# Kernel tuning notes

Measured on AMD Instinct MI355X. Metric: run time of the kernel, lower is better.

Reference implementation:

```python
import jax, jax.numpy as jnp
import numpy as np


def _masked_var(x, mask):
    # unbiased variance (torch.var default, ddof=1) over entries where mask==1
    cnt = jnp.sum(mask)
    mean = jnp.sum(x * mask) / jnp.maximum(cnt, 1.0)
    return jnp.sum(mask * (x - mean) ** 2) / jnp.maximum(cnt - 1.0, 1.0)


def setup_inputs() -> dict:
    key = jax.random.key(0)
    ks = jax.random.split(key, 9)
    B, N, F = 4, 8192, 64
    points = jax.random.normal(ks[0], (B, N, 3), dtype=jnp.float32)
    features = jax.random.normal(ks[1], (B, N, F), dtype=jnp.float32)
    leaf_mask = jax.random.randint(ks[2], (B, N), 0, 2).astype(bool)
    W1 = jax.random.normal(ks[3], (64, F + 3), dtype=jnp.float32) * 0.05
    b1 = jax.random.normal(ks[4], (64,), dtype=jnp.float32) * 0.05
    W2 = jax.random.normal(ks[5], (32, 64), dtype=jnp.float32) * 0.05
    b2 = jax.random.normal(ks[6], (32,), dtype=jnp.float32) * 0.05
    W3 = jax.random.normal(ks[7], (1, 32), dtype=jnp.float32) * 0.05
    b3 = jax.random.normal(ks[8], (1,), dtype=jnp.float32) * 0.05
    return {"points": points, "features": features, "leaf_mask": leaf_mask,
            "W1": W1, "b1": b1, "W2": W2, "b2": b2, "W3": W3, "b3": b3}


def reference(points, features, leaf_mask, W1, b1, W2, b2, W3, b3):
    # NOTE: in the original Torch code combined_feat = [feat(F), xyz(3), var(1)]
    # (length F+4) is truncated to expected_input_dim = F+3, so the kNN feature
    # variance is provably dropped. The MLP input is exactly [feat, xyz].
    B, N, _ = points.shape

    def mlp(x):  # x: [N, F+3]
        h = jax.nn.relu(x @ W1.T + b1)
        h = jax.nn.relu(h @ W2.T + b2)
        return jax.nn.sigmoid(h @ W3.T + b3)[:, 0]

    def per_batch(pts, feats, mask):
        maskf = mask.astype(pts.dtype)
        x = jnp.concatenate([feats, pts], axis=-1)  # [N, F+3]
        scores = mlp(x) * maskf  # non-leaf points stay 0
        n_leaf = jnp.sum(maskf)
        scores = jnp.where(n_leaf < 10.0, jnp.zeros_like(scores), scores)

        # separation confidence
        clarity = _masked_var(scores, maskf)
        sel = scores > 0.7
        cnt = jnp.sum(sel.astype(jnp.int32))
        idx = jnp.arange(N)
        order = jnp.argsort(jnp.where(sel, idx, N + idx))  # selected first, in order
        g = pts[order]  # [N,3]
        d = jnp.linalg.norm(g[1:] - g[:-1], axis=1)  # consecutive boundary-point dists
        pair_mask = (jnp.arange(N - 1) < cnt - 1).astype(pts.dtype)
        dvar = _masked_var(d, pair_mask)
        cont = jnp.clip(1.0 / (dvar + 1e-8), 0.0, 1.0)
        cont = jnp.where(cnt > 5, cont, 0.0)
        conf = jnp.clip(clarity * cont, 0.0, 1.0)
        conf = jnp.where(n_leaf == 0.0, 0.0, conf)
        return scores, conf

    boundary_prob, separation_confidence = jax.vmap(per_batch)(points, features, leaf_mask)
    return boundary_prob, features, separation_confidence
```

## Files before the change

### kernel.cpp

```cpp
#include <hip/hip_runtime.h>
#include <math.h>

#define NB 4
#define NPTS 8192
#define OUT_FEAT_OFF 32768
#define OUT_CONF_OFF (32768 + 2097152)

__device__ __forceinline__ float blockReduceSum256(float v) {
    __shared__ float sred[4];
#pragma unroll
    for (int o = 32; o > 0; o >>= 1) v += __shfl_down(v, o, 64);
    const int w = threadIdx.x >> 6, l = threadIdx.x & 63;
    __syncthreads();
    if (l == 0) sred[w] = v;
    __syncthreads();
    return sred[0] + sred[1] + sred[2] + sred[3];
}

__global__ __launch_bounds__(256) void fused_kernel(
    const float* __restrict__ pts,
    const float* __restrict__ feats,
    const int* __restrict__ mask,
    const float* __restrict__ W1,
    const float* __restrict__ b1,
    const float* __restrict__ W2,
    const float* __restrict__ b2,
    const float* __restrict__ W3,
    const float* __restrict__ b3,
    float* __restrict__ out,
    int* __restrict__ counters,
    float* __restrict__ wsf)
{
    __shared__ float sX[64 * 68];
    __shared__ float sH[3 * 64 * 36];
    __shared__ int sflag;
    __shared__ int cnts[256];

    const int t = threadIdx.x;
    const int ln = t & 63;
    const int q = __builtin_amdgcn_readfirstlane(t >> 6);

    {
        const float4* fsrc = (const float4*)feats + (size_t)blockIdx.x * 1024;
        float4* fdst = (float4*)(out + OUT_FEAT_OFF) + (size_t)blockIdx.x * 1024;
#pragma unroll
        for (int i = 0; i < 4; ++i) {
            const int e = i * 256 + t;
            const float4 v = fsrc[e];
            fdst[e] = v;
            *(float4*)&sX[(e >> 4) * 68 + (e & 15) * 4] = v;
        }
    }
    __syncthreads();

    const int p = blockIdx.x * 64 + ln;

    float4 xv[16];
#pragma unroll
    for (int kc = 0; kc < 16; ++kc)
        xv[kc] = *(const float4*)&sX[ln * 68 + kc * 4];
    const float px = pts[(size_t)p * 3 + 0];
    const float py = pts[(size_t)p * 3 + 1];
    const float pz = pts[(size_t)p * 3 + 2];

    const int jq = q * 16;
    float h1[16];
#pragma unroll
    for (int jj = 0; jj < 16; ++jj) {
        const float* wr = W1 + (size_t)(jq + jj) * 67;
        float a = b1[jq + jj];
#pragma unroll
        for (int kc = 0; kc < 16; ++kc) {
            a = fmaf(xv[kc].x, wr[4 * kc + 0], a);
            a = fmaf(xv[kc].y, wr[4 * kc + 1], a);
            a = fmaf(xv[kc].z, wr[4 * kc + 2], a);
            a = fmaf(xv[kc].w, wr[4 * kc + 3], a);
        }
        a = fmaf(px, wr[64], a);
        a = fmaf(py, wr[65], a);
        a = fmaf(pz, wr[66], a);
        h1[jj] = fmaxf(a, 0.f);
    }

    float p2[32];
#pragma unroll
    for (int j = 0; j < 32; ++j) {
        const float* wr = W2 + (size_t)j * 64 + jq;
        float a = 0.f;
#pragma unroll
        for (int kk = 0; kk < 16; ++kk) a = fmaf(h1[kk], wr[kk], a);
        p2[j] = a;
    }

    if (q != 0) {
        float* dst = &sH[(size_t)((q - 1) * 64 + ln) * 36];
#pragma unroll
        for (int m = 0; m < 8; ++m) {
            float4 v;
            v.x = p2[4 * m + 0]; v.y = p2[4 * m + 1];
            v.z = p2[4 * m + 2]; v.w = p2[4 * m + 3];
            *(float4*)&dst[4 * m] = v;
        }
    }
    __syncthreads();

    if (q == 0) {
#pragma unroll
        for (int qq = 0; qq < 3; ++qq) {
            const float* src = &sH[(size_t)(qq * 64 + ln) * 36];
#pragma unroll
            for (int m = 0; m < 8; ++m) {
                const float4 v = *(const float4*)&src[4 * m];
                p2[4 * m + 0] += v.x; p2[4 * m + 1] += v.y;
                p2[4 * m + 2] += v.z; p2[4 * m + 3] += v.w;
            }
        }
        float z = b3[0];
#pragma unroll
        for (int j = 0; j < 32; ++j)
            z = fmaf(fmaxf(p2[j] + b2[j], 0.f), W3[j], z);
        float sc = 1.0f / (1.0f + expf(-z));
        if (mask[p] == 0) sc = 0.0f;
        out[p] = sc;
    }

    const int batch = blockIdx.x >> 7;
    __syncthreads();
    if (t == 0) {
        const int old = __hip_atomic_fetch_add(&counters[batch], 1,
                                               __ATOMIC_ACQ_REL,
                                               __HIP_MEMORY_SCOPE_AGENT);
        sflag = (old == 127);
    }
    __syncthreads();
    if (!sflag) return;
    __builtin_amdgcn_fence(__ATOMIC_ACQUIRE, "agent");

    float* scores = out + (size_t)batch * NPTS;
    const float* P = pts + (size_t)batch * NPTS * 3;
    const int* M = mask + (size_t)batch * NPTS;
    float* g = wsf + (size_t)batch * 40960;
    float* dd = g + 3 * NPTS;

    float s[32];
    unsigned int mbits = 0;
#pragma unroll
    for (int i = 0; i < 8; ++i) {
        const float4 s4 = ((const float4*)scores)[t * 8 + i];
        s[4*i+0] = s4.x; s[4*i+1] = s4.y; s[4*i+2] = s4.z; s[4*i+3] = s4.w;
        const int4 m4 = ((const int4*)M)[t * 8 + i];
        mbits |= (m4.x != 0 ? 1u : 0u) << (4*i+0);
        mbits |= (m4.y != 0 ? 1u : 0u) << (4*i+1);
        mbits |= (m4.z != 0 ? 1u : 0u) << (4*i+2);
        mbits |= (m4.w != 0 ? 1u : 0u) << (4*i+3);
    }

    float ss = 0.f;
#pragma unroll
    for (int i = 0; i < 32; ++i) ss += s[i];
    const float nleaf = blockReduceSum256((float)__popc(mbits));
    const float ssum = blockReduceSum256(ss);

    if (nleaf < 10.0f) {
        const float4 z4 = {0.f, 0.f, 0.f, 0.f};
#pragma unroll
        for (int i = 0; i < 8; ++i) ((float4*)scores)[t * 8 + i] = z4;
        if (t == 0) out[OUT_CONF_OFF + batch] = 0.0f;
        return;
    }

    const float mean = ssum / fmaxf(nleaf, 1.0f);
    float vs = 0.f;
#pragma unroll
    for (int i = 0; i < 32; ++i) {
        if (mbits & (1u << i)) {
            const float d0 = s[i] - mean;
            vs += d0 * d0;
        }
    }
    const float clarity = blockReduceSum256(vs) / fmaxf(nleaf - 1.0f, 1.0f);

    int c0 = 0;
#pragma unroll
    for (int i = 0; i < 32; ++i) c0 += (s[i] > 0.7f);
    cnts[t] = c0;
    __syncthreads();
    for (int off = 1; off < 256; off <<= 1) {
        const int v = cnts[t];
        const int a = (t >= off) ? cnts[t - off] : 0;
        __syncthreads();
        cnts[t] = v + a;
        __syncthreads();
    }
    const int cnt = cnts[255];
    int pos = cnts[t] - c0;
#pragma unroll
    for (int i = 0; i < 32; ++i) {
        if (s[i] > 0.7f) {
            const int idx = t * 32 + i;
            g[3 * pos + 0] = P[3 * idx + 0];
            g[3 * pos + 1] = P[3 * idx + 1];
            g[3 * pos + 2] = P[3 * idx + 2];
            ++pos;
        }
    }
    __syncthreads();

    const int npair = cnt - 1;
    float dsum = 0.f;
    for (int i = t; i < npair; i += 256) {
        const float ax = g[3 * i + 0] - g[3 * i + 3];
        const float ay = g[3 * i + 1] - g[3 * i + 4];
        const float az = g[3 * i + 2] - g[3 * i + 5];
        const float d0 = sqrtf(ax * ax + ay * ay + az * az);
        dd[i] = d0;
        dsum += d0;
    }
    const float dtot = blockReduceSum256(dsum);
    const float npf = (float)npair;
    const float dmean = dtot / fmaxf(npf, 1.0f);
    float dv = 0.f;
    for (int i = t; i < npair; i += 256) {
        const float e = dd[i] - dmean;
        dv += e * e;
    }
    const float dvar = blockReduceSum256(dv) / fmaxf(npf - 1.0f, 1.0f);

    float cont = fminf(fmaxf(1.0f / (dvar + 1e-8f), 0.0f), 1.0f);
    if (!(cnt > 5)) cont = 0.0f;
    const float conf = fminf(fmaxf(clarity * cont, 0.0f), 1.0f);
    if (t == 0) out[OUT_CONF_OFF + batch] = conf;
}

extern "C" void kernel_launch(void* const* d_in, const int* in_sizes, int n_in,
                              void* d_out, int out_size, void* d_ws, size_t ws_size,
                              hipStream_t stream) {
    const float* points   = (const float*)d_in[0];
    const float* features = (const float*)d_in[1];
    const int*   leafmask = (const int*)d_in[2];
    const float* W1 = (const float*)d_in[3];
    const float* b1 = (const float*)d_in[4];
    const float* W2 = (const float*)d_in[5];
    const float* b2 = (const float*)d_in[6];
    const float* W3 = (const float*)d_in[7];
    const float* b3 = (const float*)d_in[8];
    float* out = (float*)d_out;
    int* counters = (int*)d_ws;
    float* wsf = (float*)d_ws + 64;

    (void)hipMemsetAsync(d_ws, 0, 64, stream);
    fused_kernel<<<512, 256, 0, stream>>>(
        points, features, leafmask, W1, b1, W2, b2, W3, b3, out, counters, wsf);
}
```

Before: 117.0 us.

## Use wave-shuffle scan, LDS distance buffer, and split FMA accumulators

The per-batch tail block's shared-memory Hillis-Steele prefix scan, which needed many __syncthreads, is replaced by a wave-level __shfl_up scan plus a small cross-wave combine. Consecutive-point distances now go to LDS, reusing the MLP staging buffer, instead of a global workspace. The MLP dot products use several independent accumulators to shorten FMA dependency chains. The point coordinate loads are hoisted ahead of the feature copy, and launch bounds now request two blocks per SM. Splitting the accumulators changes the floating-point summation order, and the occupancy hint may limit how many registers the compiler can use.

New measurement: 109.6 us. -6.3%, faster.

```diff
diff --git a/kernel.cpp b/kernel.cpp
--- a/kernel.cpp
+++ b/kernel.cpp
@@ -17,7 +17,7 @@
     return sred[0] + sred[1] + sred[2] + sred[3];
 }
 
-__global__ __launch_bounds__(256) void fused_kernel(
+__global__ __launch_bounds__(256, 2) void fused_kernel(
     const float* __restrict__ pts,
     const float* __restrict__ feats,
     const int* __restrict__ mask,
@@ -31,14 +31,21 @@
     int* __restrict__ counters,
     float* __restrict__ wsf)
 {
-    __shared__ float sX[64 * 68];
-    __shared__ float sH[3 * 64 * 36];
+    __shared__ float smem[11264];
+    float* const sX = smem;
+    float* const sH = smem + 64 * 68;
     __shared__ int sflag;
-    __shared__ int cnts[256];
+    __shared__ int swt[4];
 
     const int t = threadIdx.x;
     const int ln = t & 63;
     const int q = __builtin_amdgcn_readfirstlane(t >> 6);
+
+    const int p = blockIdx.x * 64 + ln;
+
+    const float px = pts[(size_t)p * 3 + 0];
+    const float py = pts[(size_t)p * 3 + 1];
+    const float pz = pts[(size_t)p * 3 + 2];
 
     {
         const float4* fsrc = (const float4*)feats + (size_t)blockIdx.x * 1024;
@@ -53,43 +60,41 @@
     }
     __syncthreads();
 
-    const int p = blockIdx.x * 64 + ln;
-
     float4 xv[16];
 #pragma unroll
     for (int kc = 0; kc < 16; ++kc)
         xv[kc] = *(const float4*)&sX[ln * 68 + kc * 4];
-    const float px = pts[(size_t)p * 3 + 0];
-    const float py = pts[(size_t)p * 3 + 1];
-    const float pz = pts[(size_t)p * 3 + 2];
 
     const int jq = q * 16;
     float h1[16];
 #pragma unroll
     for (int jj = 0; jj < 16; ++jj) {
-        const float* wr = W1 + (size_t)(jq + jj) * 67;
-        float a = b1[jq + jj];
+        const float* __restrict__ wr = W1 + (size_t)(jq + jj) * 67;
+        float a0 = b1[jq + jj], a1 = 0.f, a2 = 0.f, a3 = 0.f;
 #pragma unroll
         for (int kc = 0; kc < 16; ++kc) {
-            a = fmaf(xv[kc].x, wr[4 * kc + 0], a);
-            a = fmaf(xv[kc].y, wr[4 * kc + 1], a);
-            a = fmaf(xv[kc].z, wr[4 * kc + 2], a);
-            a = fmaf(xv[kc].w, wr[4 * kc + 3], a);
-        }
-        a = fmaf(px, wr[64], a);
-        a = fmaf(py, wr[65], a);
-        a = fmaf(pz, wr[66], a);
-        h1[jj] = fmaxf(a, 0.f);
+            a0 = fmaf(xv[kc].x, wr[4 * kc + 0], a0);
+            a1 = fmaf(xv[kc].y, wr[4 * kc + 1], a1);
+            a2 = fmaf(xv[kc].z, wr[4 * kc + 2], a2);
+            a3 = fmaf(xv[kc].w, wr[4 * kc + 3], a3);
+        }
+        a0 = fmaf(px, wr[64], a0);
+        a1 = fmaf(py, wr[65], a1);
+        a2 = fmaf(pz, wr[66], a2);
+        h1[jj] = fmaxf((a0 + a1) + (a2 + a3), 0.f);
     }
 
     float p2[32];
 #pragma unroll
     for (int j = 0; j < 32; ++j) {
-        const float* wr = W2 + (size_t)j * 64 + jq;
-        float a = 0.f;
-#pragma unroll
-        for (int kk = 0; kk < 16; ++kk) a = fmaf(h1[kk], wr[kk], a);
-        p2[j] = a;
+        const float* __restrict__ wr = W2 + (size_t)j * 64 + jq;
+        float a0 = 0.f, a1 = 0.f;
+#pragma unroll
+        for (int kk = 0; kk < 8; ++kk) {
+            a0 = fmaf(h1[2 * kk + 0], wr[2 * kk + 0], a0);
+            a1 = fmaf(h1[2 * kk + 1], wr[2 * kk + 1], a1);
+        }
+        p2[j] = a0 + a1;
     }
 
     if (q != 0) {
@@ -140,7 +145,6 @@
     const float* P = pts + (size_t)batch * NPTS * 3;
     const int* M = mask + (size_t)batch * NPTS;
     float* g = wsf + (size_t)batch * 40960;
-    float* dd = g + 3 * NPTS;
 
     float s[32];
     unsigned int mbits = 0;
@@ -183,17 +187,23 @@
     int c0 = 0;
 #pragma unroll
     for (int i = 0; i < 32; ++i) c0 += (s[i] > 0.7f);
-    cnts[t] = c0;
-    __syncthreads();
-    for (int off = 1; off < 256; off <<= 1) {
-        const int v = cnts[t];
-        const int a = (t >= off) ? cnts[t - off] : 0;
-        __syncthreads();
-        cnts[t] = v + a;
-        __syncthreads();
-    }
-    const int cnt = cnts[255];
-    int pos = cnts[t] - c0;
+    int incl = c0;
+#pragma unroll
+    for (int o = 1; o < 64; o <<= 1) {
+        const int u = __shfl_up(incl, o, 64);
+        if (ln >= o) incl += u;
+    }
+    const int w = t >> 6;
+    if (ln == 63) swt[w] = incl;
+    __syncthreads();
+    int woff = 0, cnt = 0;
+#pragma unroll
+    for (int i = 0; i < 4; ++i) {
+        const int wv = swt[i];
+        if (i < w) woff += wv;
+        cnt += wv;
+    }
+    int pos = woff + (incl - c0);
 #pragma unroll
     for (int i = 0; i < 32; ++i) {
         if (s[i] > 0.7f) {
@@ -206,22 +216,25 @@
     }
     __syncthreads();
 
+    float* const ddl = smem;
     const int npair = cnt - 1;
     float dsum = 0.f;
+#pragma unroll 4
     for (int i = t; i < npair; i += 256) {
         const float ax = g[3 * i + 0] - g[3 * i + 3];
         const float ay = g[3 * i + 1] - g[3 * i + 4];
         const float az = g[3 * i + 2] - g[3 * i + 5];
         const float d0 = sqrtf(ax * ax + ay * ay + az * az);
-        dd[i] = d0;
+        ddl[i] = d0;
         dsum += d0;
     }
     const float dtot = blockReduceSum256(dsum);
     const float npf = (float)npair;
     const float dmean = dtot / fmaxf(npf, 1.0f);
     float dv = 0.f;
+#pragma unroll 4
     for (int i = t; i < npair; i += 256) {
-        const float e = dd[i] - dmean;
+        const float e = ddl[i] - dmean;
         dv += e * e;
     }
     const float dvar = blockReduceSum256(dv) / fmaxf(npf - 1.0f, 1.0f);
```
